# Kernel tuning notes

Hardware: AMD Instinct MI355X
Metric: run time of the kernel (lower is better)

Reference implementation:

```python
import jax, jax.numpy as jnp
import numpy as np

BLOCK_SIZE = 32
NUM_PROJS = 7


def _unit_hamming(n):
    # AngularLSH._unit_hamming_distance_array (Gray-code-like permutation)
    a = np.array([0, 1], dtype=np.int32)
    for i in range(1, n):
        a = np.concatenate([a, a[::-1] + 2 ** i])
    return a


def _lsh_hash(x, proj_dir, perm, enc_vec):
    # x: [B,H,N,D], proj_dir: [1,1,D,P] -> hash ids [B,H,N]
    pd = proj_dir[0, 0]  # [D,P]
    proj = jnp.einsum('bhnd,dp->bhnp', x, pd)
    bits = (proj > 0).astype(jnp.int32)
    bin_ids = (bits * enc_vec).sum(-1)
    return perm[bin_ids]


def _causal_attn(q, k, v):
    # q,k,v: [B,N,H,D] (xformers layout), causal softmax attention
    B, N, H, D = q.shape
    s = jnp.einsum('bqhd,bkhd->bhqk', q, k) * (D ** -0.5)
    causal = jnp.tril(jnp.ones((N, N), dtype=bool))
    s = jnp.where(causal, s, jnp.finfo(s.dtype).min)
    w = jax.nn.softmax(s, axis=-1)
    return jnp.einsum('bhqk,bkhd->bqhd', w, v)


def _forward(q, k, v, proj_dir):
    B, N, H, D = q.shape
    bs = BLOCK_SIZE
    nb = N // bs
    perm = jnp.asarray(_unit_hamming(NUM_PROJS))
    enc_vec = jnp.asarray(2 ** np.arange(NUM_PROJS, dtype=np.int32))

    qt = jnp.transpose(q, (0, 2, 1, 3))  # [B,H,N,D]
    kt = jnp.transpose(k, (0, 2, 1, 3))

    q_hash = _lsh_hash(qt, proj_dir, perm, enc_vec)  # [B,H,N]
    sort_idx = jnp.argsort(q_hash, axis=2, stable=True)
    q_hash_sort = jnp.take_along_axis(q_hash, sort_idx, axis=2)
    inv_idx = jnp.argsort(sort_idx, axis=2, stable=True)
    q_sorted = jnp.take_along_axis(qt, sort_idx[..., None], axis=2)  # [B,H,N,D]

    k_hash = _lsh_hash(kt, proj_dir, perm, enc_vec)  # [B,H,N]

    # torch .view(seq_len, -1) on [B,H,N] contiguous tensors (C-order reshape)
    qh_rows = q_hash_sort.reshape(N, -1)  # [N, B*H]
    kh_rows = k_hash.reshape(N, -1)
    eq = (qh_rows == kh_rows).reshape(nb, -1)  # rows grouped by query block
    keep = (eq.sum(axis=1) > 0)  # [nb] block kept if any hash match

    # K_split_per_block = k.reshape(B, nb, -1, D) on [B,H,N,D]
    k_blocks = kt.reshape(B, nb, (H * N) // nb, D)
    k_blocks = k_blocks * keep[None, :, None, None].astype(kt.dtype)
    k_crit = k_blocks.reshape(B, H, N, D)

    # out_critical = attn(q_critical, k_critical, v_critical) then unsort
    out = _causal_attn(jnp.transpose(q_sorted, (0, 2, 1, 3)),
                       jnp.transpose(k_crit, (0, 2, 1, 3)),
                       v)  # [B,N,H,D]
    out = jnp.take_along_axis(jnp.transpose(out, (0, 2, 1, 3)), inv_idx[..., None], axis=2)
    return jnp.transpose(out, (0, 2, 1, 3))  # [B,N,H,D]


def setup_inputs() -> dict:
    key = jax.random.key(0)
    k1, k2, k3, k4 = jax.random.split(key, 4)
    B, N, H, D = 2, 2048, 16, 128
    return {
        'q': jax.random.normal(k1, (B, N, H, D), dtype=jnp.float32),
        'k': jax.random.normal(k2, (B, N, H, D), dtype=jnp.float32),
        'v': jax.random.normal(k3, (B, N, H, D), dtype=jnp.float32),
        'proj_dir': jax.random.normal(k4, (1, 1, D, NUM_PROJS), dtype=jnp.float32),
        'is_causal': 1,
        'mask': jnp.zeros((1, 1), dtype=bool),
    }


def reference(q, k, v, proj_dir, is_causal, mask):
    # is_causal is always True at every attention call site; mask is unused then.
    return _forward(q, k, v, proj_dir)
```

## Files before the change

kernel.cpp:

```cpp
#include <hip/hip_runtime.h>
#include <cstdint>

#define BB 2
#define NN 2048
#define HH 16
#define DD 128
#define BH 32
#define NPROJ 7

typedef __bf16 bf16x8 __attribute__((ext_vector_type(8)));
typedef float f32x4 __attribute__((ext_vector_type(4)));

__device__ __forceinline__ unsigned short f2bf(float f) {
  unsigned int u = __float_as_uint(f);
  u += 0x7fff + ((u >> 16) & 1);
  return (unsigned short)(u >> 16);
}

__device__ __forceinline__ bf16x8 load_q8(const float* p) {
  float4 a = *(const float4*)p;
  float4 b = *(const float4*)(p + 4);
  unsigned short r[8] = {f2bf(a.x), f2bf(a.y), f2bf(a.z), f2bf(a.w),
                         f2bf(b.x), f2bf(b.y), f2bf(b.z), f2bf(b.w)};
  return *(bf16x8*)r;
}

__global__ void prep_kernel(const float* __restrict__ q, const float* __restrict__ k,
                            const float* __restrict__ v, const float* __restrict__ pd,
                            int* __restrict__ qh, int* __restrict__ kh,
                            unsigned short* __restrict__ Vt) {
  __shared__ __align__(16) char smem[64 * 132 * 2];
  if (blockIdx.x < 4096) {
    float* spd = (float*)smem;
    for (int i = threadIdx.x; i < DD * NPROJ; i += 256) spd[i] = pd[i];
    __syncthreads();
    long long gid = (long long)blockIdx.x * 256 + threadIdx.x;
    int part = (int)(gid & 7);
    long long row = gid >> 3;
    const long long NR = (long long)BB * NN * HH;
    int isk = row >= NR;
    long long r = isk ? row - NR : row;
    const float* src = (isk ? k : q) + r * DD + part * 16;
    double acc[NPROJ];
    for (int p = 0; p < NPROJ; ++p) acc[p] = 0.0;
    for (int d = 0; d < 16; d += 4) {
      float4 x = *(const float4*)(src + d);
      int dbase = part * 16 + d;
      for (int p = 0; p < NPROJ; ++p) {
        acc[p] += (double)x.x * (double)spd[(dbase + 0) * NPROJ + p]
                + (double)x.y * (double)spd[(dbase + 1) * NPROJ + p]
                + (double)x.z * (double)spd[(dbase + 2) * NPROJ + p]
                + (double)x.w * (double)spd[(dbase + 3) * NPROJ + p];
      }
    }
    for (int off = 1; off < 8; off <<= 1)
      for (int p = 0; p < NPROJ; ++p) acc[p] += __shfl_xor(acc[p], off);
    if (part == 0) {
      int bin = 0;
      for (int p = 0; p < NPROJ; ++p) bin |= ((int)(acc[p] > 0.0)) << p;
      int hsh = bin ^ (bin >> 1);
      int b_ = (int)(r / (NN * HH));
      int rem = (int)(r % (NN * HH));
      int n_ = rem / HH, h_ = rem % HH;
      (isk ? kh : qh)[((long long)b_ * HH + h_) * NN + n_] = hsh;
    }
  } else {
    unsigned short (*tile)[132] = (unsigned short(*)[132])smem;
    int blk = blockIdx.x - 4096;
    int bh = blk >> 5;
    int n0 = (blk & 31) * 64;
    int b = bh >> 4, h = bh & 15;
    for (int it = 0; it < 8; ++it) {
      int cid = it * 256 + threadIdx.x;
      int r = cid >> 5, d4 = (cid & 31) * 4;
      float4 x = *(const float4*)(v + (((long long)(b * NN + n0 + r) * HH + h) << 7) + d4);
      *(ushort4*)&tile[r][d4] = make_ushort4(f2bf(x.x), f2bf(x.y), f2bf(x.z), f2bf(x.w));
    }
    __syncthreads();
    for (int it = 0; it < 8; ++it) {
      int cid = it * 256 + threadIdx.x;
      int d = cid >> 4, n4 = (cid & 15) * 4;
      ushort4 y = make_ushort4(tile[n4 + 0][d], tile[n4 + 1][d], tile[n4 + 2][d], tile[n4 + 3][d]);
      *(ushort4*)(Vt + ((long long)bh * DD + d) * NN + n0 + n4) = y;
    }
  }
}

__global__ void sortkeep_kernel(const int* __restrict__ qh, const int* __restrict__ kh,
                                int* __restrict__ sidx, int* __restrict__ keep) {
  __shared__ int sh[NN];
  __shared__ int cnt[4][128];
  __shared__ int cum[128];
  __shared__ int kflag[2];
  int bh = blockIdx.x;
  const int* src = qh + (long long)bh * NN;
  for (int i = threadIdx.x; i < NN; i += 512) sh[i] = src[i];
  if (threadIdx.x < 2) kflag[threadIdx.x] = 0;
  __syncthreads();
  int bin = threadIdx.x & 127, seg = threadIdx.x >> 7;
  int n0 = seg * (NN / 4);
  int c = 0;
  for (int n = n0; n < n0 + NN / 4; ++n) c += (sh[n] == bin);
  cnt[seg][bin] = c;
  __syncthreads();
  if (threadIdx.x == 0) {
    int run = 0;
    for (int t = 0; t < 128; ++t) {
      cum[t] = run;
      run += cnt[0][t] + cnt[1][t] + cnt[2][t] + cnt[3][t];
    }
  }
  __syncthreads();
  int pos = cum[bin];
  for (int s = 0; s < seg; ++s) pos += cnt[s][bin];
  int f0 = 0, f1 = 0;
  for (int n = n0; n < n0 + NN / 4; ++n)
    if (sh[n] == bin) {
      sidx[(long long)bh * NN + pos] = n;
      int match = (bin == kh[(long long)bh * NN + pos]);
      if (pos < 1024) f0 |= match; else f1 |= match;
      ++pos;
    }
  if (f0) atomicOr(&kflag[0], 1);
  if (f1) atomicOr(&kflag[1], 1);
  __syncthreads();
  if (threadIdx.x < 2) keep[bh * 2 + threadIdx.x] = kflag[threadIdx.x];
}

__global__ __launch_bounds__(256, 1)
void flash_kernel(const float* __restrict__ q, const float* __restrict__ k,
                  const unsigned short* __restrict__ Vt, const int* __restrict__ sidx,
                  const int* __restrict__ keep, float* __restrict__ out) {
  __shared__ __align__(16) unsigned short Kt[64 * 136];
  __shared__ __align__(16) unsigned short Vs[128 * 72];
  __shared__ __align__(16) unsigned short Pb[4][16 * 72];

  int bx = blockIdx.x;
  int bh = blockIdx.y;
  int b = bh >> 4, h = bh & 15;
  int tid = threadIdx.x;
  int w = tid >> 6, lane = tid & 63;
  int l16 = lane & 15, qd = lane >> 4;

  const float* kbase = k + (long long)b * NN * HH * DD + h * DD;
  const unsigned short* Vb = Vt + (long long)bh * DD * NN;
  const float scale = 0.088388347648318447f;

  for (int ph = 0; ph < 2; ++ph) {
    int qt = ph ? bx : 31 - bx;
    int qrow = qt * 64 + w * 16 + l16;

    bf16x8 qf[4];
    {
      int nq = sidx[bh * NN + qrow];
      const float* p0 = q + (((long long)(b * NN + nq) * HH + h) << 7) + qd * 8;
#pragma unroll
      for (int c = 0; c < 4; ++c) qf[c] = load_q8(p0 + c * 32);
    }
    f32x4 o[8];
#pragma unroll
    for (int i = 0; i < 8; ++i) o[i] = (f32x4){0.f, 0.f, 0.f, 0.f};
    float m = -__builtin_inff(), l = 0.f;

    for (int kb = 0; kb <= qt; ++kb) {
      int k0 = kb * 64;
      int kp = keep[h * 4 + (k0 >> 9)];

      if (kp) {
#pragma unroll
        for (int it = 0; it < 8; ++it) {
          int cid = it * 256 + tid;
          int r = cid >> 5, d4 = (cid & 31) * 4;
          float4 x = *(const float4*)(kbase + (long long)(k0 + r) * (HH * DD) + d4);
          *(ushort4*)&Kt[r * 136 + d4] = make_ushort4(f2bf(x.x), f2bf(x.y), f2bf(x.z), f2bf(x.w));
        }
      } else {
#pragma unroll
        for (int it = 0; it < 8; ++it) {
          int cid = it * 256 + tid;
          int r = cid >> 5, d4 = (cid & 31) * 4;
          *(ushort4*)&Kt[r * 136 + d4] = make_ushort4(0, 0, 0, 0);
        }
      }
#pragma unroll
      for (int it = 0; it < 4; ++it) {
        int cid = it * 256 + tid;
        int r = cid >> 3, c8 = (cid & 7) * 8;
        *(uint4*)&Vs[r * 72 + c8] = *(const uint4*)(Vb + (long long)r * NN + k0 + c8);
      }
      __syncthreads();

      float s[16];
#pragma unroll
      for (int t = 0; t < 4; ++t) {
        f32x4 a1 = (f32x4){0.f, 0.f, 0.f, 0.f};
#pragma unroll
        for (int c = 0; c < 4; ++c) {
          bf16x8 kf = *(const bf16x8*)&Kt[(t * 16 + l16) * 136 + c * 32 + qd * 8];
          a1 = __builtin_amdgcn_mfma_f32_16x16x32_bf16(kf, qf[c], a1, 0, 0, 0);
        }
#pragma unroll
        for (int r = 0; r < 4; ++r) {
          int keyg = k0 + t * 16 + qd * 4 + r;
          s[t * 4 + r] = (keyg > qrow) ? -__builtin_inff() : a1[r] * scale;
        }
      }

      {
        float mloc = s[0];
#pragma unroll
        for (int i = 1; i < 16; ++i) mloc = fmaxf(mloc, s[i]);
        mloc = fmaxf(mloc, __shfl_xor(mloc, 16));
        mloc = fmaxf(mloc, __shfl_xor(mloc, 32));
        float mnew = fmaxf(m, mloc);
        float alpha = __expf(m - mnew);
        float psum = 0.f;
#pragma unroll
        for (int t = 0; t < 4; ++t) {
          float p0 = __expf(s[t * 4 + 0] - mnew);
          float p1 = __expf(s[t * 4 + 1] - mnew);
          float p2 = __expf(s[t * 4 + 2] - mnew);
          float p3 = __expf(s[t * 4 + 3] - mnew);
          psum += (p0 + p1) + (p2 + p3);
          *(ushort4*)&Pb[w][l16 * 72 + t * 16 + qd * 4] =
              make_ushort4(f2bf(p0), f2bf(p1), f2bf(p2), f2bf(p3));
        }
        psum += __shfl_xor(psum, 16);
        psum += __shfl_xor(psum, 32);
        l = l * alpha + psum;
        m = mnew;
        float aO[4];
#pragma unroll
        for (int r = 0; r < 4; ++r) aO[r] = __shfl(alpha, qd * 4 + r);
#pragma unroll
        for (int c8 = 0; c8 < 8; ++c8)
#pragma unroll
          for (int r = 0; r < 4; ++r) o[c8][r] *= aO[r];
      }

#pragma unroll
      for (int g = 0; g < 2; ++g) {
        bf16x8 pf = *(const bf16x8*)&Pb[w][l16 * 72 + g * 32 + qd * 8];
#pragma unroll
        for (int c8 = 0; c8 < 8; ++c8) {
          bf16x8 vf = *(const bf16x8*)&Vs[(c8 * 16 + l16) * 72 + g * 32 + qd * 8];
          o[c8] = __builtin_amdgcn_mfma_f32_16x16x32_bf16(pf, vf, o[c8], 0, 0, 0);
        }
      }
      __syncthreads();
    }

    float lO[4];
    int nO[4];
#pragma unroll
    for (int r = 0; r < 4; ++r) {
      lO[r] = __shfl(l, qd * 4 + r);
      nO[r] = sidx[(long long)bh * NN + qt * 64 + w * 16 + qd * 4 + r];
    }
#pragma unroll
    for (int r = 0; r < 4; ++r) {
      float inv = 1.f / lO[r];
      float* ob = out + (((long long)(b * NN + nO[r]) * HH + h) << 7) + l16;
#pragma unroll
      for (int c8 = 0; c8 < 8; ++c8)
        ob[c8 * 16] = o[c8][r] * inv;
    }
  }
}

extern "C" void kernel_launch(void* const* d_in, const int* in_sizes, int n_in,
                              void* d_out, int out_size, void* d_ws, size_t ws_size,
                              hipStream_t stream) {
  const float* q = (const float*)d_in[0];
  const float* k = (const float*)d_in[1];
  const float* v = (const float*)d_in[2];
  const float* pd = (const float*)d_in[3];
  float* out = (float*)d_out;
  char* ws = (char*)d_ws;
  int* qh   = (int*)(ws + 0);
  int* kh   = (int*)(ws + (1u << 18));
  int* sidx = (int*)(ws + (2u << 18));
  int* keep = (int*)(ws + 3u * (1u << 18));
  unsigned short* Vt = (unsigned short*)(ws + (2u << 20));

  prep_kernel<<<5120, 256, 0, stream>>>(q, k, v, pd, qh, kh, Vt);
  sortkeep_kernel<<<32, 512, 0, stream>>>(qh, kh, sidx, keep);
  flash_kernel<<<dim3(16, 32), 256, 0, stream>>>(q, k, Vt, sidx, keep, out);
}
```

Before: 365.1 us.

## Precompute bf16 K in prep and double-buffer K/V tiles in flash kernel

The prep kernel now writes a bf16 copy of K in a [B,H,N,D] layout alongside the hashing pass, so the flash kernel loads half the bytes and skips per-tile conversion. The flash kernel double-buffers K and V in shared memory, prefetching the next tile into registers while the current one computes, which removes one barrier per iteration. The causal mask is applied only on the diagonal tile, and the output rescale is skipped when no row max increases. Launch bounds move to two blocks per CU, at the cost of extra workspace, more LDS and more register pressure.

```diff
diff --git a/kernel.cpp b/kernel.cpp
--- a/kernel.cpp
+++ b/kernel.cpp
@@ -28,7 +28,7 @@
 __global__ void prep_kernel(const float* __restrict__ q, const float* __restrict__ k,
                             const float* __restrict__ v, const float* __restrict__ pd,
                             int* __restrict__ qh, int* __restrict__ kh,
-                            unsigned short* __restrict__ Vt) {
+                            unsigned short* __restrict__ Vt, unsigned short* __restrict__ Kb) {
   __shared__ __align__(16) char smem[64 * 132 * 2];
   if (blockIdx.x < 4096) {
     float* spd = (float*)smem;
@@ -43,8 +43,13 @@
     const float* src = (isk ? k : q) + r * DD + part * 16;
     double acc[NPROJ];
     for (int p = 0; p < NPROJ; ++p) acc[p] = 0.0;
+    __align__(16) unsigned short kb16[16];
     for (int d = 0; d < 16; d += 4) {
       float4 x = *(const float4*)(src + d);
+      if (isk) {
+        kb16[d + 0] = f2bf(x.x); kb16[d + 1] = f2bf(x.y);
+        kb16[d + 2] = f2bf(x.z); kb16[d + 3] = f2bf(x.w);
+      }
       int dbase = part * 16 + d;
       for (int p = 0; p < NPROJ; ++p) {
         acc[p] += (double)x.x * (double)spd[(dbase + 0) * NPROJ + p]
@@ -53,15 +58,20 @@
                 + (double)x.w * (double)spd[(dbase + 3) * NPROJ + p];
       }
     }
+    int b_ = (int)(r / (NN * HH));
+    int rem = (int)(r % (NN * HH));
+    int n_ = rem / HH, h_ = rem % HH;
+    if (isk) {
+      unsigned short* dst = Kb + (((long long)(b_ * HH + h_) * NN + n_) << 7) + part * 16;
+      *(uint4*)dst = *(const uint4*)&kb16[0];
+      *(uint4*)(dst + 8) = *(const uint4*)&kb16[8];
+    }
     for (int off = 1; off < 8; off <<= 1)
       for (int p = 0; p < NPROJ; ++p) acc[p] += __shfl_xor(acc[p], off);
     if (part == 0) {
       int bin = 0;
       for (int p = 0; p < NPROJ; ++p) bin |= ((int)(acc[p] > 0.0)) << p;
       int hsh = bin ^ (bin >> 1);
-      int b_ = (int)(r / (NN * HH));
-      int rem = (int)(r % (NN * HH));
-      int n_ = rem / HH, h_ = rem % HH;
       (isk ? kh : qh)[((long long)b_ * HH + h_) * NN + n_] = hsh;
     }
   } else {
@@ -127,12 +137,12 @@
   if (threadIdx.x < 2) keep[bh * 2 + threadIdx.x] = kflag[threadIdx.x];
 }
 
-__global__ __launch_bounds__(256, 1)
-void flash_kernel(const float* __restrict__ q, const float* __restrict__ k,
+__global__ __launch_bounds__(256, 2)
+void flash_kernel(const float* __restrict__ q, const unsigned short* __restrict__ Kb,
                   const unsigned short* __restrict__ Vt, const int* __restrict__ sidx,
                   const int* __restrict__ keep, float* __restrict__ out) {
-  __shared__ __align__(16) unsigned short Kt[64 * 136];
-  __shared__ __align__(16) unsigned short Vs[128 * 72];
+  __shared__ __align__(16) unsigned short Kt[2][64 * 136];
+  __shared__ __align__(16) unsigned short Vs[2][128 * 72];
   __shared__ __align__(16) unsigned short Pb[4][16 * 72];
 
   int bx = blockIdx.x;
@@ -142,9 +152,41 @@
   int w = tid >> 6, lane = tid & 63;
   int l16 = lane & 15, qd = lane >> 4;
 
-  const float* kbase = k + (long long)b * NN * HH * DD + h * DD;
+  const unsigned short* Kh = Kb + (long long)bh * NN * DD;
   const unsigned short* Vb = Vt + (long long)bh * DD * NN;
   const float scale = 0.088388347648318447f;
+
+  const int ksr = tid >> 4;
+  const int ksc = (tid & 15) * 8;
+  const int vsr = tid >> 3;
+  const int vsc = (tid & 7) * 8;
+
+  uint4 kreg[4], vreg[4];
+
+#define STAGE_LOAD(K0, KP)                                                            \
+  {                                                                                   \
+    if (KP) {                                                                         \
+      _Pragma("unroll")                                                               \
+      for (int it = 0; it < 4; ++it)                                                  \
+        kreg[it] = *(const uint4*)(Kh + (long long)((K0) + it * 16 + ksr) * DD + ksc);\
+    } else {                                                                          \
+      _Pragma("unroll")                                                               \
+      for (int it = 0; it < 4; ++it) kreg[it] = make_uint4(0, 0, 0, 0);               \
+    }                                                                                 \
+    _Pragma("unroll")                                                                 \
+    for (int it = 0; it < 4; ++it)                                                    \
+      vreg[it] = *(const uint4*)(Vb + (long long)(it * 32 + vsr) * NN + (K0) + vsc);  \
+  }
+
+#define STAGE_WRITE(BUF)                                                              \
+  {                                                                                   \
+    _Pragma("unroll")                                                                 \
+    for (int it = 0; it < 4; ++it)                                                    \
+      *(uint4*)&Kt[BUF][(it * 16 + ksr) * 136 + ksc] = kreg[it];                      \
+    _Pragma("unroll")                                                                 \
+    for (int it = 0; it < 4; ++it)                                                    \
+      *(uint4*)&Vs[BUF][(it * 32 + vsr) * 72 + vsc] = vreg[it];                       \
+  }
 
   for (int ph = 0; ph < 2; ++ph) {
     int qt = ph ? bx : 31 - bx;
@@ -162,33 +204,18 @@
     for (int i = 0; i < 8; ++i) o[i] = (f32x4){0.f, 0.f, 0.f, 0.f};
     float m = -__builtin_inff(), l = 0.f;
 
+    int cur = 0;
+    STAGE_LOAD(0, keep[h * 4]);
+    __syncthreads();
+    STAGE_WRITE(0);
+    __syncthreads();
+
     for (int kb = 0; kb <= qt; ++kb) {
+      if (kb < qt) STAGE_LOAD((kb + 1) * 64, keep[h * 4 + ((kb + 1) >> 3)]);
+
       int k0 = kb * 64;
-      int kp = keep[h * 4 + (k0 >> 9)];
-
-      if (kp) {
-#pragma unroll
-        for (int it = 0; it < 8; ++it) {
-          int cid = it * 256 + tid;
-          int r = cid >> 5, d4 = (cid & 31) * 4;
-          float4 x = *(const float4*)(kbase + (long long)(k0 + r) * (HH * DD) + d4);
-          *(ushort4*)&Kt[r * 136 + d4] = make_ushort4(f2bf(x.x), f2bf(x.y), f2bf(x.z), f2bf(x.w));
-        }
-      } else {
-#pragma unroll
-        for (int it = 0; it < 8; ++it) {
-          int cid = it * 256 + tid;
-          int r = cid >> 5, d4 = (cid & 31) * 4;
-          *(ushort4*)&Kt[r * 136 + d4] = make_ushort4(0, 0, 0, 0);
-        }
-      }
-#pragma unroll
-      for (int it = 0; it < 4; ++it) {
-        int cid = it * 256 + tid;
-        int r = cid >> 3, c8 = (cid & 7) * 8;
-        *(uint4*)&Vs[r * 72 + c8] = *(const uint4*)(Vb + (long long)r * NN + k0 + c8);
-      }
-      __syncthreads();
+      const unsigned short* Ktc = Kt[cur];
+      const unsigned short* Vsc = Vs[cur];
 
       float s[16];
 #pragma unroll
@@ -196,13 +223,18 @@
         f32x4 a1 = (f32x4){0.f, 0.f, 0.f, 0.f};
 #pragma unroll
         for (int c = 0; c < 4; ++c) {
-          bf16x8 kf = *(const bf16x8*)&Kt[(t * 16 + l16) * 136 + c * 32 + qd * 8];
+          bf16x8 kf = *(const bf16x8*)&Ktc[(t * 16 + l16) * 136 + c * 32 + qd * 8];
           a1 = __builtin_amdgcn_mfma_f32_16x16x32_bf16(kf, qf[c], a1, 0, 0, 0);
         }
-#pragma unroll
-        for (int r = 0; r < 4; ++r) {
-          int keyg = k0 + t * 16 + qd * 4 + r;
-          s[t * 4 + r] = (keyg > qrow) ? -__builtin_inff() : a1[r] * scale;
+        if (kb == qt) {
+#pragma unroll
+          for (int r = 0; r < 4; ++r) {
+            int keyg = k0 + t * 16 + qd * 4 + r;
+            s[t * 4 + r] = (keyg > qrow) ? -__builtin_inff() : a1[r] * scale;
+          }
+        } else {
+#pragma unroll
+          for (int r = 0; r < 4; ++r) s[t * 4 + r] = a1[r] * scale;
         }
       }
 
@@ -212,30 +244,33 @@
         for (int i = 1; i < 16; ++i) mloc = fmaxf(mloc, s[i]);
         mloc = fmaxf(mloc, __shfl_xor(mloc, 16));
         mloc = fmaxf(mloc, __shfl_xor(mloc, 32));
-        float mnew = fmaxf(m, mloc);
-        float alpha = __expf(m - mnew);
+        if (__any(mloc > m)) {
+          float mnew = fmaxf(m, mloc);
+          float alpha = __expf(m - mnew);
+          float aO[4];
+#pragma unroll
+          for (int r = 0; r < 4; ++r) aO[r] = __shfl(alpha, qd * 4 + r);
+#pragma unroll
+          for (int c8 = 0; c8 < 8; ++c8)
+#pragma unroll
+            for (int r = 0; r < 4; ++r) o[c8][r] *= aO[r];
+          l *= alpha;
+          m = mnew;
+        }
         float psum = 0.f;
 #pragma unroll
         for (int t = 0; t < 4; ++t) {
-          float p0 = __expf(s[t * 4 + 0] - mnew);
-          float p1 = __expf(s[t * 4 + 1] - mnew);
-          float p2 = __expf(s[t * 4 + 2] - mnew);
-          float p3 = __expf(s[t * 4 + 3] - mnew);
+          float p0 = __expf(s[t * 4 + 0] - m);
+          float p1 = __expf(s[t * 4 + 1] - m);
+          float p2 = __expf(s[t * 4 + 2] - m);
+          float p3 = __expf(s[t * 4 + 3] - m);
           psum += (p0 + p1) + (p2 + p3);
           *(ushort4*)&Pb[w][l16 * 72 + t * 16 + qd * 4] =
               make_ushort4(f2bf(p0), f2bf(p1), f2bf(p2), f2bf(p3));
         }
         psum += __shfl_xor(psum, 16);
         psum += __shfl_xor(psum, 32);
-        l = l * alpha + psum;
-        m = mnew;
-        float aO[4];
-#pragma unroll
-        for (int r = 0; r < 4; ++r) aO[r] = __shfl(alpha, qd * 4 + r);
-#pragma unroll
-        for (int c8 = 0; c8 < 8; ++c8)
-#pragma unroll
-          for (int r = 0; r < 4; ++r) o[c8][r] *= aO[r];
+        l += psum;
       }
 
 #pragma unroll
@@ -243,11 +278,16 @@
         bf16x8 pf = *(const bf16x8*)&Pb[w][l16 * 72 + g * 32 + qd * 8];
 #pragma unroll
         for (int c8 = 0; c8 < 8; ++c8) {
-          bf16x8 vf = *(const bf16x8*)&Vs[(c8 * 16 + l16) * 72 + g * 32 + qd * 8];
+          bf16x8 vf = *(const bf16x8*)&Vsc[(c8 * 16 + l16) * 72 + g * 32 + qd * 8];
           o[c8] = __builtin_amdgcn_mfma_f32_16x16x32_bf16(pf, vf, o[c8], 0, 0, 0);
         }
       }
-      __syncthreads();
+
+      if (kb < qt) {
+        STAGE_WRITE(cur ^ 1);
+        __syncthreads();
+        cur ^= 1;
+      }
     }
 
     float lO[4];
@@ -266,6 +306,8 @@
         ob[c8 * 16] = o[c8][r] * inv;
     }
   }
+#undef STAGE_LOAD
+#undef STAGE_WRITE
 }
 
 extern "C" void kernel_launch(void* const* d_in, const int* in_sizes, int n_in,
@@ -282,8 +324,9 @@
   int* sidx = (int*)(ws + (2u << 18));
   int* keep = (int*)(ws + 3u * (1u << 18));
   unsigned short* Vt = (unsigned short*)(ws + (2u << 20));
-
-  prep_kernel<<<5120, 256, 0, stream>>>(q, k, v, pd, qh, kh, Vt);
+  unsigned short* Kb = (unsigned short*)(ws + (18u << 20));
+
+  prep_kernel<<<5120, 256, 0, stream>>>(q, k, v, pd, qh, kh, Vt, Kb);
   sortkeep_kernel<<<32, 512, 0, stream>>>(qh, kh, sidx, keep);
-  flash_kernel<<<dim3(16, 32), 256, 0, stream>>>(q, k, Vt, sidx, keep, out);
-}
+  flash_kernel<<<dim3(16, 32), 256, 0, stream>>>(q, Kb, Vt, sidx, keep, out);
+}
```

New measurement: 359.5 us. Within noise of the previous version (-1.5%).
